# Kernel optimization log

Hardware: AMD Instinct MI355X
Metric: run time of the kernel (lower is better)

## Reference

```python
import jax, jax.numpy as jnp
import numpy as np

H = 8          # num_heads
CHUNK = 68     # tokens_per_chunk = blocks_per_chunk(4) * tokens_per_block(17)
EPS = 1e-5


def _layer_norm(t, w, b):
    m = t.mean(-1, keepdims=True)
    v = t.var(-1, keepdims=True)
    return (t - m) / jnp.sqrt(v + EPS) * w + b


def _forward(tokens, embedding, Wq, bq, Wk, bk, Wv, bv, Wg, bg, Wo, bo,
             gn_w, gn_b, ln1_w, ln1_b, ln2_w, ln2_b, w1, b1, w2, b2):
    B, S = tokens.shape
    L, D, _ = Wq.shape
    dh = D // H
    n_chunks = S // CHUNK

    x = embedding[tokens]  # [B,S,D]

    # per-head decay gammas (standard RetNet)
    gamma = 1.0 - 2.0 ** (-5.0 - jnp.arange(H, dtype=jnp.float32))  # [H]

    # rotary relative-position tables (absolute positions, fresh state n=0)
    pos = jnp.arange(S, dtype=jnp.float32)
    inv = 1.0 / (10000.0 ** (jnp.arange(0, dh, 2, dtype=jnp.float32) / dh))
    ang = pos[:, None] * inv[None, :]                      # [S, dh/2]
    cs = jnp.concatenate([jnp.cos(ang)] * 2, -1)[None, :, None, :]  # [1,S,1,dh]
    sn = jnp.concatenate([jnp.sin(ang)] * 2, -1)[None, :, None, :]

    def rot(t):  # t: [B,S,H,dh]
        t1, t2 = jnp.split(t, 2, axis=-1)
        return t * cs + jnp.concatenate([-t2, t1], -1) * sn

    # chunkwise decay structures
    idx = jnp.arange(CHUNK, dtype=jnp.float32)
    expo = idx[:, None] - idx[None, :]
    Dmask = jnp.where(expo >= 0, gamma[:, None, None] ** expo[None], 0.0)  # [H,C,C]
    cross_dec = gamma[None, :] ** (idx[:, None] + 1.0)          # [C,H]
    k_dec = gamma[None, :] ** (CHUNK - 1.0 - idx[:, None])      # [C,H]
    chunk_dec = gamma ** CHUNK                                  # [H]

    for l in range(L):
        h = _layer_norm(x, ln1_w[l], ln1_b[l])
        q = rot((h @ Wq[l] + bq[l]).reshape(B, S, H, dh))
        k = rot((h @ Wk[l] + bk[l]).reshape(B, S, H, dh)) * (dh ** -0.5)
        v = (h @ Wv[l] + bv[l]).reshape(B, S, H, dh)
        # split into chunks, scan carries the per-head KV state [B,H,dh,dh]
        qc = q.reshape(B, n_chunks, CHUNK, H, dh).transpose(1, 0, 2, 3, 4)
        kc = k.reshape(B, n_chunks, CHUNK, H, dh).transpose(1, 0, 2, 3, 4)
        vc = v.reshape(B, n_chunks, CHUNK, H, dh).transpose(1, 0, 2, 3, 4)

        def step(state, qkv):
            qq, kk, vv = qkv  # each [B,C,H,dh]
            inner = jnp.einsum('bihd,bjhd->bhij', qq, kk) * Dmask
            out = jnp.einsum('bhij,bjhd->bihd', inner, vv)
            out = out + jnp.einsum('bihd,bhde->bihe', qq, state) * cross_dec[None, :, :, None]
            state = state * chunk_dec[None, :, None, None] + \
                jnp.einsum('bjhd,bjhe->bhde', kk * k_dec[None, :, :, None], vv)
            return state, out

        state0 = jnp.zeros((B, H, dh, dh), dtype=x.dtype)
        _, ret = jax.lax.scan(step, state0, (qc, kc, vc))
        ret = ret.transpose(1, 0, 2, 3, 4).reshape(B, S, H, dh)
        # per-head group norm
        m = ret.mean(-1, keepdims=True)
        vr = ret.var(-1, keepdims=True)
        ret = (ret - m) / jnp.sqrt(vr + EPS)
        ret = (ret * gn_w[l].reshape(H, dh) + gn_b[l].reshape(H, dh)).reshape(B, S, D)
        g = jax.nn.silu(h @ Wg[l] + bg[l])
        x = x + (g * ret) @ Wo[l] + bo[l]
        h2 = _layer_norm(x, ln2_w[l], ln2_b[l])
        x = x + jax.nn.silu(h2 @ w1[l] + b1[l]) @ w2[l] + b2[l]
    return x


def setup_inputs() -> dict:
    key = jax.random.key(0)
    B, S, D, L, FF, V = 16, 408, 512, 10, 2048, 519
    ks = jax.random.split(key, 16)
    r = lambda i, shape, s=0.02: jax.random.normal(ks[i], shape, dtype=jnp.float32) * s
    return {
        'tokens': jax.random.randint(ks[0], (B, S), 0, V, dtype=jnp.int32),
        'embedding': r(1, (V, D)),
        'Wq': r(2, (L, D, D)), 'bq': jnp.zeros((L, D), jnp.float32),
        'Wk': r(3, (L, D, D)), 'bk': jnp.zeros((L, D), jnp.float32),
        'Wv': r(4, (L, D, D)), 'bv': jnp.zeros((L, D), jnp.float32),
        'Wg': r(5, (L, D, D)), 'bg': jnp.zeros((L, D), jnp.float32),
        'Wo': r(6, (L, D, D)), 'bo': jnp.zeros((L, D), jnp.float32),
        'gn_w': jnp.ones((L, D), jnp.float32), 'gn_b': jnp.zeros((L, D), jnp.float32),
        'ln1_w': jnp.ones((L, D), jnp.float32), 'ln1_b': jnp.zeros((L, D), jnp.float32),
        'ln2_w': jnp.ones((L, D), jnp.float32), 'ln2_b': jnp.zeros((L, D), jnp.float32),
        'w1': r(7, (L, D, FF)), 'b1': jnp.zeros((L, FF), jnp.float32),
        'w2': r(8, (L, FF, D)), 'b2': jnp.zeros((L, D), jnp.float32),
    }


def reference(tokens, embedding, Wq, bq, Wk, bk, Wv, bv, Wg, bg, Wo, bo,
              gn_w, gn_b, ln1_w, ln1_b, ln2_w, ln2_b, w1, b1, w2, b2):
    return _forward(tokens, embedding, Wq, bq, Wk, bk, Wv, bv, Wg, bg, Wo, bo,
                    gn_w, gn_b, ln1_w, ln1_b, ln2_w, ln2_b, w1, b1, w2, b2)
```

## Files before the change

### kernel.cpp

```cpp
#include <hip/hip_runtime.h>
#include <hip/hip_bf16.h>

#define H 8
#define DH 64
#define DMODEL 512
#define SEQ 408
#define BATCH 16
#define NLAYER 10
#define FFDIM 2048
#define CHUNK 68
#define NCHUNK 6
#define M (BATCH*SEQ)
#define EPS 1e-5f

typedef __hip_bfloat16 bf16;
typedef unsigned short ushort_t;
typedef short bf8v __attribute__((ext_vector_type(8)));
typedef float f4v  __attribute__((ext_vector_type(4)));

static constexpr size_t QKVG_STRIDE = 2u*512*512;
static constexpr size_t QKVG_HL     = 512*512;
static constexpr size_t WO_HI = 0;
static constexpr size_t WO_LO = WO_HI + 512*512;
static constexpr size_t W1_HI = WO_LO + 512*512;
static constexpr size_t W1_LO = W1_HI + 2048*512;
static constexpr size_t W2_HI = W1_LO + 2048*512;
static constexpr size_t W2_LO = W2_HI + 512*2048;

__device__ __forceinline__ float us2f(unsigned short u){ return __uint_as_float(((unsigned)u) << 16); }
__device__ __forceinline__ unsigned short f2bfs(float f){
  __bf16 h = (__bf16)f;
  return *(unsigned short*)&h;
}
__device__ __forceinline__ void split2(float f, unsigned short& hi, unsigned short& lo){
  hi = f2bfs(f);
  lo = f2bfs(f - us2f(hi));
}

__device__ __forceinline__ int xcd_swz(int fid, int nwg){
  int q = nwg >> 3;
  return (fid & 7) * q + (fid >> 3);
}

__global__ void embed_kernel(const int* __restrict__ tokens, const float* __restrict__ emb,
                             float* __restrict__ x){
  int idx = blockIdx.x*256 + threadIdx.x;
  if (idx >= M*DMODEL) return;
  int r = idx >> 9; int d = idx & 511;
  x[idx] = emb[(size_t)tokens[r]*DMODEL + d];
}

__global__ __launch_bounds__(256) void ln_kernel(const float* __restrict__ x,
    const float* __restrict__ w, const float* __restrict__ b,
    ushort_t* __restrict__ hhi, ushort_t* __restrict__ hlo){
  __shared__ float red[8];
  int r = blockIdx.x, tid = threadIdx.x;
  size_t base = (size_t)r*DMODEL;
  float v0 = x[base + tid], v1 = x[base + tid + 256];
  float s = v0 + v1, s2 = v0*v0 + v1*v1;
  int lane = tid & 63, wv = tid >> 6;
  #pragma unroll
  for (int o = 32; o; o >>= 1){ s += __shfl_xor(s, o); s2 += __shfl_xor(s2, o); }
  if (lane == 0){ red[wv] = s; red[wv+4] = s2; }
  __syncthreads();
  float tot  = red[0]+red[1]+red[2]+red[3];
  float tot2 = red[4]+red[5]+red[6]+red[7];
  float mean = tot * (1.0f/512.0f);
  float var  = tot2 * (1.0f/512.0f) - mean*mean;
  float rinv = rsqrtf(var + EPS);
  float o0 = (v0-mean)*rinv*w[tid]     + b[tid];
  float o1 = (v1-mean)*rinv*w[tid+256] + b[tid+256];
  unsigned short hi, lo;
  split2(o0, hi, lo); hhi[base+tid] = hi; hlo[base+tid] = lo;
  split2(o1, hi, lo); hhi[base+tid+256] = hi; hlo[base+tid+256] = lo;
}

__device__ __forceinline__ void wsplit_tile(const float* __restrict__ W,
    ushort_t* __restrict__ hi, ushort_t* __restrict__ lo,
    int N, int K, int n0, int k0)
{
  __shared__ float tb[32][33];
  int tx = threadIdx.x & 31, ty = threadIdx.x >> 5;
  #pragma unroll
  for (int r = 0; r < 32; r += 8)
    tb[ty+r][tx] = W[(size_t)(k0+ty+r)*N + n0 + tx];
  __syncthreads();
  #pragma unroll
  for (int r = 0; r < 32; r += 8){
    float v = tb[tx][ty+r];
    unsigned short h, l; split2(v, h, l);
    size_t o = (size_t)(n0+ty+r)*K + k0 + tx;
    hi[o] = h; lo[o] = l;
  }
}

__global__ __launch_bounds__(256) void wsplit_qkvg_kernel(
    const float* __restrict__ Wq, const float* __restrict__ Wk,
    const float* __restrict__ Wv, const float* __restrict__ Wg,
    ushort_t* __restrict__ wsp)
{
  int z = blockIdx.z;
  const float* W = (z==0)?Wq:(z==1)?Wk:(z==2)?Wv:Wg;
  ushort_t* hi = wsp + (size_t)z*QKVG_STRIDE;
  wsplit_tile(W, hi, hi + QKVG_HL, 512, 512, blockIdx.x*32, blockIdx.y*32);
}

__global__ __launch_bounds__(256) void wsplit_ffo_kernel(
    const float* __restrict__ Wo, const float* __restrict__ w1,
    const float* __restrict__ w2, ushort_t* __restrict__ wsp)
{
  int b = blockIdx.x;
  const float* W; ushort_t* hi; int N, K, n0, k0;
  if (b < 256){
    W = Wo; hi = wsp + WO_HI; N = 512; K = 512;
    n0 = (b & 15)*32; k0 = (b >> 4)*32;
  } else if (b < 1280){
    int bb = b - 256;
    W = w1; hi = wsp + W1_HI; N = 2048; K = 512;
    n0 = (bb & 63)*32; k0 = (bb >> 6)*32;
  } else {
    int bb = b - 1280;
    W = w2; hi = wsp + W2_HI; N = 512; K = 2048;
    n0 = (bb & 15)*32; k0 = (bb >> 4)*32;
  }
  wsplit_tile(W, hi, hi + (size_t)N*K, N, K, n0, k0);
}

#define BK 32
#define LDK 40

template<int TBM, int TBN>
__global__ __launch_bounds__(256) void gemm_ps_kernel(
    const ushort_t* __restrict__ Ahi, const ushort_t* __restrict__ Alo,
    const ushort_t* __restrict__ Bhi, const ushort_t* __restrict__ Blo,
    const float* __restrict__ bias,
    const float* Cin, float* Cout, ushort_t* Co_hi, ushort_t* Co_lo,
    int N, int K, int epi)
{
  constexpr int TMi = TBM/32;
  constexpr int TNj = TBN/32;
  __shared__ __align__(16) short AsH[TBM*LDK];
  __shared__ __align__(16) short AsL[TBM*LDK];
  __shared__ __align__(16) short BsH[TBN*LDK];
  __shared__ __align__(16) short BsL[TBN*LDK];
  int tid = threadIdx.x;
  int lane = tid & 63, wave = tid >> 6;
  int wm = (wave >> 1) * (TBM/2), wn = (wave & 1) * (TBN/2);
  int l15 = lane & 15, quad = lane >> 4;

  int nwg = gridDim.x * gridDim.y;
  int fid = blockIdx.y * gridDim.x + blockIdx.x;
  int swz = xcd_swz(fid, nwg);
  int bn = (swz % gridDim.x) * TBN;
  int bm = (swz / gridDim.x) * TBM;

  f4v acc[TMi][TNj];
  #pragma unroll
  for (int i = 0; i < TMi; i++)
    #pragma unroll
    for (int j = 0; j < TNj; j++) acc[i][j] = (f4v){0.f,0.f,0.f,0.f};

  int arow, akseg, bnn, bkseg;
  if (TBM == 128){ arow = tid >> 1; akseg = (tid & 1) * 16; }
  else           { arow = tid >> 2; akseg = (tid & 3) * 8;  }
  if (TBN == 128){ bnn = tid & 127; bkseg = (tid >> 7) * 16; }
  else           { bnn = tid & 63;  bkseg = (tid >> 6) * 8;  }

  const ushort_t* aH = Ahi + (size_t)(bm + arow)*K + akseg;
  const ushort_t* aL = Alo + (size_t)(bm + arow)*K + akseg;
  const ushort_t* bH = Bhi + (size_t)(bn + bnn)*K + bkseg;
  const ushort_t* bL = Blo + (size_t)(bn + bnn)*K + bkseg;

  uint4 rAh0, rAh1, rAl0, rAl1, rBh0, rBh1, rBl0, rBl1;
#define GLOAD_PS(k0) do{ \
    rAh0 = *(const uint4*)(aH + (k0)); \
    rAl0 = *(const uint4*)(aL + (k0)); \
    if (TBM == 128){ rAh1 = *(const uint4*)(aH + (k0) + 8); \
                     rAl1 = *(const uint4*)(aL + (k0) + 8); } \
    rBh0 = *(const uint4*)(bH + (k0)); \
    rBl0 = *(const uint4*)(bL + (k0)); \
    if (TBN == 128){ rBh1 = *(const uint4*)(bH + (k0) + 8); \
                     rBl1 = *(const uint4*)(bL + (k0) + 8); } \
  }while(0)

  GLOAD_PS(0);
  const int nt = K / BK;
  for (int t = 0; t < nt; t++){
    __syncthreads();
    *(uint4*)&AsH[arow*LDK + akseg] = rAh0;
    *(uint4*)&AsL[arow*LDK + akseg] = rAl0;
    if (TBM == 128){
      *(uint4*)&AsH[arow*LDK + akseg + 8] = rAh1;
      *(uint4*)&AsL[arow*LDK + akseg + 8] = rAl1;
    }
    *(uint4*)&BsH[bnn*LDK + bkseg] = rBh0;
    *(uint4*)&BsL[bnn*LDK + bkseg] = rBl0;
    if (TBN == 128){
      *(uint4*)&BsH[bnn*LDK + bkseg + 8] = rBh1;
      *(uint4*)&BsL[bnn*LDK + bkseg + 8] = rBl1;
    }
    __syncthreads();
    if (t + 1 < nt) GLOAD_PS((t+1)*BK);
    bf8v afh[TMi], afl[TMi], bfh[TNj], bfl[TNj];
    #pragma unroll
    for (int i = 0; i < TMi; i++){
      afh[i] = *(const bf8v*)&AsH[(wm + i*16 + l15)*LDK + quad*8];
      afl[i] = *(const bf8v*)&AsL[(wm + i*16 + l15)*LDK + quad*8];
    }
    #pragma unroll
    for (int j = 0; j < TNj; j++){
      bfh[j] = *(const bf8v*)&BsH[(wn + j*16 + l15)*LDK + quad*8];
      bfl[j] = *(const bf8v*)&BsL[(wn + j*16 + l15)*LDK + quad*8];
    }
    #pragma unroll
    for (int i = 0; i < TMi; i++)
      #pragma unroll
      for (int j = 0; j < TNj; j++){
        acc[i][j] = __builtin_amdgcn_mfma_f32_16x16x32_bf16(afh[i], bfl[j], acc[i][j], 0, 0, 0);
        acc[i][j] = __builtin_amdgcn_mfma_f32_16x16x32_bf16(afl[i], bfh[j], acc[i][j], 0, 0, 0);
        acc[i][j] = __builtin_amdgcn_mfma_f32_16x16x32_bf16(afh[i], bfh[j], acc[i][j], 0, 0, 0);
      }
  }
#undef GLOAD_PS
  #pragma unroll
  for (int i = 0; i < TMi; i++){
    int m0 = bm + wm + i*16 + quad*4;
    #pragma unroll
    for (int j = 0; j < TNj; j++){
      int n = bn + wn + j*16 + l15;
      float bsv = bias[n];
      #pragma unroll
      for (int r = 0; r < 4; r++){
        int m = m0 + r;
        float c = acc[i][j][r] + bsv;
        if (epi == 1) c = c / (1.0f + expf(-c));
        if (epi == 2) c += Cin[(size_t)m*N + n];
        if (Co_hi){
          unsigned short hi, lo; split2(c, hi, lo);
          Co_hi[(size_t)m*N + n] = hi;
          Co_lo[(size_t)m*N + n] = lo;
        } else {
          Cout[(size_t)m*N + n] = c;
        }
      }
    }
  }
}

__global__ __launch_bounds__(256) void gemm_qkvg_kernel(
    const ushort_t* __restrict__ Ahi, const ushort_t* __restrict__ Alo,
    const ushort_t* __restrict__ wsp,
    const float* __restrict__ bq, const float* __restrict__ bk,
    const float* __restrict__ bv, const float* __restrict__ bg,
    float* __restrict__ qo, float* __restrict__ ko,
    float* __restrict__ vo, float* __restrict__ go)
{
  const int N = DMODEL, K = DMODEL;
  __shared__ __align__(16) short AsH[128*LDK];
  __shared__ __align__(16) short AsL[128*LDK];
  __shared__ __align__(16) short BsH[128*LDK];
  __shared__ __align__(16) short BsL[128*LDK];
  int tid = threadIdx.x;
  int lane = tid & 63, wave = tid >> 6;
  int wm = (wave >> 1) * 64, wn = (wave & 1) * 64;
  int l15 = lane & 15, quad = lane >> 4;

  int nwg = gridDim.x * gridDim.y;
  int fid = blockIdx.y * gridDim.x + blockIdx.x;
  int swz = xcd_swz(fid, nwg);
  int bx = swz % gridDim.x;
  int which = bx >> 2;
  int bn = (bx & 3) * 128;
  int bm = (swz / gridDim.x) * 128;

  const ushort_t* Bhi = wsp + (size_t)which * QKVG_STRIDE;
  const ushort_t* Blo = Bhi + QKVG_HL;
  const float* bias = (which==0) ? bq : (which==1) ? bk : (which==2) ? bv : bg;
  float* out        = (which==0) ? qo : (which==1) ? ko : (which==2) ? vo : go;

  f4v acc[4][4];
  #pragma unroll
  for (int i = 0; i < 4; i++)
    #pragma unroll
    for (int j = 0; j < 4; j++) acc[i][j] = (f4v){0.f,0.f,0.f,0.f};

  int arow = tid >> 1, akseg = (tid & 1) * 16;
  int bnn = tid & 127, bkseg = (tid >> 7) * 16;

  const ushort_t* aH = Ahi + (size_t)(bm + arow)*K + akseg;
  const ushort_t* aL = Alo + (size_t)(bm + arow)*K + akseg;
  const ushort_t* bH = Bhi + (size_t)(bn + bnn)*K + bkseg;
  const ushort_t* bL = Blo + (size_t)(bn + bnn)*K + bkseg;

  uint4 rAh0, rAh1, rAl0, rAl1, rBh0, rBh1, rBl0, rBl1;
#define GLOADQ(k0) do{ \
    rAh0 = *(const uint4*)(aH + (k0)); rAh1 = *(const uint4*)(aH + (k0) + 8); \
    rAl0 = *(const uint4*)(aL + (k0)); rAl1 = *(const uint4*)(aL + (k0) + 8); \
    rBh0 = *(const uint4*)(bH + (k0)); rBh1 = *(const uint4*)(bH + (k0) + 8); \
    rBl0 = *(const uint4*)(bL + (k0)); rBl1 = *(const uint4*)(bL + (k0) + 8); \
  }while(0)

  GLOADQ(0);
  const int nt = K / BK;
  for (int t = 0; t < nt; t++){
    __syncthreads();
    *(uint4*)&AsH[arow*LDK + akseg]     = rAh0;
    *(uint4*)&AsH[arow*LDK + akseg + 8] = rAh1;
    *(uint4*)&AsL[arow*LDK + akseg]     = rAl0;
    *(uint4*)&AsL[arow*LDK + akseg + 8] = rAl1;
    *(uint4*)&BsH[bnn*LDK + bkseg] = rBh0; *(uint4*)&BsH[bnn*LDK + bkseg + 8] = rBh1;
    *(uint4*)&BsL[bnn*LDK + bkseg] = rBl0; *(uint4*)&BsL[bnn*LDK + bkseg + 8] = rBl1;
    __syncthreads();
    if (t + 1 < nt) GLOADQ((t+1)*BK);
    bf8v afh[4], afl[4], bfh[4], bfl[4];
    #pragma unroll
    for (int i = 0; i < 4; i++){
      afh[i] = *(const bf8v*)&AsH[(wm + i*16 + l15)*LDK + quad*8];
      afl[i] = *(const bf8v*)&AsL[(wm + i*16 + l15)*LDK + quad*8];
      bfh[i] = *(const bf8v*)&BsH[(wn + i*16 + l15)*LDK + quad*8];
      bfl[i] = *(const bf8v*)&BsL[(wn + i*16 + l15)*LDK + quad*8];
    }
    #pragma unroll
    for (int i = 0; i < 4; i++)
      #pragma unroll
      for (int j = 0; j < 4; j++){
        acc[i][j] = __builtin_amdgcn_mfma_f32_16x16x32_bf16(afh[i], bfl[j], acc[i][j], 0, 0, 0);
        acc[i][j] = __builtin_amdgcn_mfma_f32_16x16x32_bf16(afl[i], bfh[j], acc[i][j], 0, 0, 0);
        acc[i][j] = __builtin_amdgcn_mfma_f32_16x16x32_bf16(afh[i], bfh[j], acc[i][j], 0, 0, 0);
      }
  }
#undef GLOADQ
  #pragma unroll
  for (int i = 0; i < 4; i++){
    int m0 = bm + wm + i*16 + quad*4;
    #pragma unroll
    for (int j = 0; j < 4; j++){
      int n = bn + wn + j*16 + l15;
      float bsv = bias[n];
      #pragma unroll
      for (int r = 0; r < 4; r++){
        int m = m0 + r;
        float c = acc[i][j][r] + bsv;
        if (which == 3) c = c / (1.0f + expf(-c));
        out[(size_t)m*N + n] = c;
      }
    }
  }
}

__global__ void rope_kernel(float* __restrict__ q, float* __restrict__ k){
  int idx = blockIdx.x*256 + threadIdx.x;
  if (idx >= M*256) return;
  int r = idx >> 8, p = idx & 255;
  int hh = p >> 5, i = p & 31;
  int s = r % SEQ;
  float inv = powf(10000.0f, -(float)(2*i) * (1.0f/64.0f));
  float ang = (float)s * inv;
  float sn, c; sincosf(ang, &sn, &c);
  size_t base = (size_t)r*DMODEL + hh*64 + i;
  float q1 = q[base], q2 = q[base+32];
  q[base]    = q1*c - q2*sn;
  q[base+32] = q2*c + q1*sn;
  float k1 = k[base], k2 = k[base+32];
  const float sc = 0.125f;
  k[base]    = (k1*c - k2*sn)*sc;
  k[base+32] = (k2*c + k1*sn)*sc;
}

__global__ __launch_bounds__(256) void ret_chunkkv_kernel(
    const float* __restrict__ k, const float* __restrict__ v, float* __restrict__ Ast)
{
  __shared__ __align__(16) float kT[DH][CHUNK];
  __shared__ __align__(16) float vs[CHUNK][DH];
  __shared__ float gpw[CHUNK];
  int tid = threadIdx.x;
  int c = blockIdx.x % NCHUNK;
  int bh = blockIdx.x / NCHUNK;
  int hh = bh & 7, b = bh >> 3;
  float gamma = 1.0f - exp2f(-5.0f - (float)hh);
  if (tid < CHUNK) gpw[tid] = powf(gamma, (float)(CHUNK-1-tid));
  size_t rowbase = ((size_t)(b*SEQ + c*CHUNK))*DMODEL + hh*DH;
  for (int e = tid; e < CHUNK*DH; e += 256){
    int i = e >> 6, d = e & 63;
    size_t g = rowbase + (size_t)i*DMODEL + d;
    kT[d][i] = k[g];
    vs[i][d] = v[g];
  }
  __syncthreads();
  float* A = Ast + (size_t)blockIdx.x * (DH*DH);
  for (int e = tid; e < DH*16; e += 256){
    int d = e >> 4, q4 = (e & 15) * 4;
    float4 a4 = {0,0,0,0};
    for (int j = 0; j < CHUNK; j++){
      float kj = kT[d][j] * gpw[j];
      float4 v4 = *(const float4*)&vs[j][q4];
      a4.x += kj*v4.x; a4.y += kj*v4.y; a4.z += kj*v4.z; a4.w += kj*v4.w;
    }
    *(float4*)&A[d*DH + q4] = a4;
  }
}

__global__ __launch_bounds__(256) void ret_scan_kernel(float* __restrict__ Ast)
{
  int bh = blockIdx.x, hh = bh & 7;
  float gamma = 1.0f - exp2f(-5.0f - (float)hh);
  float chdec = powf(gamma, (float)CHUNK);
  int tid = threadIdx.x;
  float4 run[4];
  #pragma unroll
  for (int t = 0; t < 4; t++) run[t] = (float4){0,0,0,0};
  size_t base = (size_t)bh * NCHUNK * (DH*DH) + (size_t)tid*16;
  for (int c = 0; c < NCHUNK; c++){
    float4* slot = (float4*)(Ast + base + (size_t)c*(DH*DH));
    float4 a[4];
    #pragma unroll
    for (int t = 0; t < 4; t++) a[t] = slot[t];
    #pragma unroll
    for (int t = 0; t < 4; t++) slot[t] = run[t];
    #pragma unroll
    for (int t = 0; t < 4; t++){
      run[t].x = run[t].x*chdec + a[t].x;
      run[t].y = run[t].y*chdec + a[t].y;
      run[t].z = run[t].z*chdec + a[t].z;
      run[t].w = run[t].w*chdec + a[t].w;
    }
  }
}

__global__ __launch_bounds__(256) void ret_out_kernel(
    const float* __restrict__ q, const float* __restrict__ k, const float* __restrict__ v,
    const float* __restrict__ Ast, float* __restrict__ ret)
{
  __shared__ __align__(16) float qs[CHUNK][DH];
  __shared__ __align__(16) float kT[DH][CHUNK];
  __shared__ __align__(16) float vs[CHUNK][DH];
  __shared__ __align__(16) float sts[DH*DH];
  __shared__ float inner[34][CHUNK];
  __shared__ float gpw[CHUNK];
  int tid = threadIdx.x;
  int c = blockIdx.x % NCHUNK;
  int bh = blockIdx.x / NCHUNK;
  int hh = bh & 7, b = bh >> 3;
  float gamma = 1.0f - exp2f(-5.0f - (float)hh);
  if (tid < CHUNK) gpw[tid] = powf(gamma, (float)tid);
  size_t rowbase = ((size_t)(b*SEQ + c*CHUNK))*DMODEL + hh*DH;
  for (int e = tid; e < CHUNK*DH; e += 256){
    int i = e >> 6, d = e & 63;
    size_t g = rowbase + (size_t)i*DMODEL + d;
    qs[i][d] = q[g];
    kT[d][i] = k[g];
    vs[i][d] = v[g];
  }
  const float* st = Ast + (size_t)blockIdx.x * (DH*DH);
  for (int e = tid*4; e < DH*DH; e += 1024)
    *(float4*)&sts[e] = *(const float4*)&st[e];
  __syncthreads();
  for (int p = 0; p < 2; p++){
    int i0 = p*34;
    for (int e = tid; e < 34*CHUNK; e += 256){
      int ii = e / CHUNK, j = e - ii*CHUNK;
      int i = i0 + ii;
      float val = 0.0f;
      if (j <= i){
        float dot = 0.0f;
        #pragma unroll 16
        for (int d = 0; d < DH; d++) dot += qs[i][d] * kT[d][j];
        val = dot * gpw[i-j];
      }
      inner[ii][j] = val;
    }
    __syncthreads();
    for (int e = tid; e < 34*16; e += 256){
      int ii = e >> 4, q4 = (e & 15) * 4;
      int i = i0 + ii;
      float4 o4 = {0,0,0,0};
      for (int j = 0; j <= i; j++){
        float w = inner[ii][j];
        float4 v4 = *(const float4*)&vs[j][q4];
        o4.x += w*v4.x; o4.y += w*v4.y; o4.z += w*v4.z; o4.w += w*v4.w;
      }
      float4 c4 = {0,0,0,0};
      #pragma unroll 8
      for (int e2 = 0; e2 < DH; e2++){
        float qv = qs[i][e2];
        float4 s4 = *(const float4*)&sts[e2*DH + q4];
        c4.x += qv*s4.x; c4.y += qv*s4.y; c4.z += qv*s4.z; c4.w += qv*s4.w;
      }
      float cd = gpw[i] * gamma;
      size_t ob = rowbase + (size_t)i*DMODEL + q4;
      float4 o; o.x = o4.x + cd*c4.x; o.y = o4.y + cd*c4.y;
      o.z = o4.z + cd*c4.z; o.w = o4.w + cd*c4.w;
      *(float4*)&ret[ob] = o;
    }
    __syncthreads();
  }
}

__global__ __launch_bounds__(512) void gnorm_gate_kernel(const float* __restrict__ ret,
    const float* __restrict__ g, const float* __restrict__ gnw, const float* __restrict__ gnb,
    ushort_t* __restrict__ ohi, ushort_t* __restrict__ olo)
{
  int r = blockIdx.x, tid = threadIdx.x;
  size_t idx = (size_t)r*DMODEL + tid;
  float val = ret[idx];
  float s = val, s2 = val*val;
  #pragma unroll
  for (int o = 32; o; o >>= 1){ s += __shfl_xor(s, o); s2 += __shfl_xor(s2, o); }
  float mean = s * (1.0f/64.0f);
  float var  = s2 * (1.0f/64.0f) - mean*mean;
  float y = (val - mean) * rsqrtf(var + EPS);
  y = y * gnw[tid] + gnb[tid];
  y = y * g[idx];
  unsigned short hi, lo; split2(y, hi, lo);
  ohi[idx] = hi; olo[idx] = lo;
}

__global__ void outwrite_kernel(const float* __restrict__ x, float* __restrict__ out){
  int idx = blockIdx.x*256 + threadIdx.x;
  if (idx < M*DMODEL) out[idx] = x[idx];
}

extern "C" void kernel_launch(void* const* d_in, const int* in_sizes, int n_in,
                              void* d_out, int out_size, void* d_ws, size_t ws_size,
                              hipStream_t stream)
{
  (void)in_sizes; (void)n_in; (void)out_size; (void)ws_size;
  const int*   tokens = (const int*)d_in[0];
  const float* emb  = (const float*)d_in[1];
  const float* Wq = (const float*)d_in[2];  const float* bq = (const float*)d_in[3];
  const float* Wk = (const float*)d_in[4];  const float* bk = (const float*)d_in[5];
  const float* Wv = (const float*)d_in[6];  const float* bv = (const float*)d_in[7];
  const float* Wg = (const float*)d_in[8];  const float* bg = (const float*)d_in[9];
  const float* Wo = (const float*)d_in[10]; const float* bo = (const float*)d_in[11];
  const float* gnw = (const float*)d_in[12]; const float* gnb = (const float*)d_in[13];
  const float* ln1w = (const float*)d_in[14]; const float* ln1b = (const float*)d_in[15];
  const float* ln2w = (const float*)d_in[16]; const float* ln2b = (const float*)d_in[17];
  const float* w1 = (const float*)d_in[18]; const float* b1 = (const float*)d_in[19];
  const float* w2 = (const float*)d_in[20]; const float* b2 = (const float*)d_in[21];

  const size_t MD = (size_t)M*DMODEL;
  float* xf = (float*)d_ws;
  float* qf = xf + MD;
  float* kf = qf + MD;
  float* vf = kf + MD;
  float* gf = vf + MD;
  float* rf = gf + MD;
  ushort_t* h_hi = (ushort_t*)(rf + MD);
  ushort_t* h_lo = h_hi + MD;
  float* Ast = (float*)h_hi;
  ushort_t* rg_hi = h_hi;
  ushort_t* rg_lo = h_lo;
  ushort_t* ff_hi = (ushort_t*)qf;
  ushort_t* ff_lo = (ushort_t*)vf;
  ushort_t* wsp = (ushort_t*)rf;

  embed_kernel<<<(M*DMODEL)/256, 256, 0, stream>>>(tokens, emb, xf);

  dim3 gqkvg(16, M/128);
  dim3 g64(DMODEL/64, M/64);
  dim3 gff(FFDIM/128, M/128);
  dim3 gsplit4(16, 16, 4);
  for (int l = 0; l < NLAYER; l++){
    const size_t wO = (size_t)l*DMODEL*DMODEL;
    const size_t bO = (size_t)l*DMODEL;
    const size_t w1O = (size_t)l*DMODEL*FFDIM;
    const size_t b1O = (size_t)l*FFDIM;
    wsplit_qkvg_kernel<<<gsplit4, 256, 0, stream>>>(Wq + wO, Wk + wO, Wv + wO, Wg + wO, wsp);
    ln_kernel<<<M, 256, 0, stream>>>(xf, ln1w + bO, ln1b + bO, h_hi, h_lo);
    gemm_qkvg_kernel<<<gqkvg, 256, 0, stream>>>(h_hi, h_lo, wsp,
        bq + bO, bk + bO, bv + bO, bg + bO,
        qf, kf, vf, gf);
    rope_kernel<<<M, 256, 0, stream>>>(qf, kf);
    ret_chunkkv_kernel<<<BATCH*H*NCHUNK, 256, 0, stream>>>(kf, vf, Ast);
    ret_scan_kernel<<<BATCH*H, 256, 0, stream>>>(Ast);
    ret_out_kernel<<<BATCH*H*NCHUNK, 256, 0, stream>>>(qf, kf, vf, Ast, rf);
    gnorm_gate_kernel<<<M, 512, 0, stream>>>(rf, gf, gnw + bO, gnb + bO, rg_hi, rg_lo);
    wsplit_ffo_kernel<<<2304, 256, 0, stream>>>(Wo + wO, w1 + w1O, w2 + w1O, wsp);
    gemm_ps_kernel<64,64><<<g64, 256, 0, stream>>>(rg_hi, rg_lo,
        wsp + WO_HI, wsp + WO_LO, bo + bO, xf, xf, nullptr, nullptr, DMODEL, DMODEL, 2);
    ln_kernel<<<M, 256, 0, stream>>>(xf, ln2w + bO, ln2b + bO, h_hi, h_lo);
    gemm_ps_kernel<128,128><<<gff, 256, 0, stream>>>(h_hi, h_lo,
        wsp + W1_HI, wsp + W1_LO, b1 + b1O, nullptr, nullptr, ff_hi, ff_lo, FFDIM, DMODEL, 1);
    gemm_ps_kernel<64,64><<<g64, 256, 0, stream>>>(ff_hi, ff_lo,
        wsp + W2_HI, wsp + W2_LO, b2 + bO, xf, xf, nullptr, nullptr, DMODEL, FFDIM, 2);
  }
  outwrite_kernel<<<(M*DMODEL)/256, 256, 0, stream>>>(xf, (float*)d_out);
}
```

Measured before the change: 4.145 ms.

## Stage GEMM tiles via direct global-to-LDS loads with double buffering

The split-bf16 GEMM kernels (QKVG and the generic projection GEMM) now copy operand tiles straight from global memory into double-buffered LDS using global_load_lds 16-byte transfers. This replaces the register-staged loads and the second barrier per K step. All these GEMMs also move to one 64x128 tile shape without LDS padding, with launch grids updated to match. The aim is to overlap the next tile's load with the MFMA work and save VGPRs and LDS store instructions. The risks are LDS bank conflicts from the unpadded rows, different occupancy and wave counts per GEMM, and needing correct vmcnt waits before the single barrier.

```diff
diff --git a/kernel.cpp b/kernel.cpp
--- a/kernel.cpp
+++ b/kernel.cpp
@@ -35,6 +35,12 @@
 __device__ __forceinline__ void split2(float f, unsigned short& hi, unsigned short& lo){
   hi = f2bfs(f);
   lo = f2bfs(f - us2f(hi));
+}
+
+typedef const __attribute__((address_space(1))) unsigned int* gas_ptr;
+typedef __attribute__((address_space(3))) unsigned int* las_ptr;
+__device__ __forceinline__ void gld16(const void* g, void* l){
+  __builtin_amdgcn_global_load_lds((gas_ptr)g, (las_ptr)l, 16, 0, 0);
 }
 
 __device__ __forceinline__ int xcd_swz(int fid, int nwg){
@@ -127,9 +133,16 @@
 }
 
 #define BK 32
-#define LDK 40
-
-template<int TBM, int TBN>
+
+#define STAGE_PS(buf, kofs) do{ \
+    gld16(aHp + (kofs), &AsH[buf][tid*8]); \
+    gld16(aLp + (kofs), &AsL[buf][tid*8]); \
+    gld16(bHp + (kofs), &BsH[buf][tid*8]); \
+    gld16(bLp + (kofs), &BsL[buf][tid*8]); \
+    gld16(bHp2 + (kofs), &BsH[buf][tid*8 + 2048]); \
+    gld16(bLp2 + (kofs), &BsL[buf][tid*8 + 2048]); \
+  }while(0)
+
 __global__ __launch_bounds__(256) void gemm_ps_kernel(
     const ushort_t* __restrict__ Ahi, const ushort_t* __restrict__ Alo,
     const ushort_t* __restrict__ Bhi, const ushort_t* __restrict__ Blo,
@@ -137,96 +150,66 @@
     const float* Cin, float* Cout, ushort_t* Co_hi, ushort_t* Co_lo,
     int N, int K, int epi)
 {
-  constexpr int TMi = TBM/32;
-  constexpr int TNj = TBN/32;
-  __shared__ __align__(16) short AsH[TBM*LDK];
-  __shared__ __align__(16) short AsL[TBM*LDK];
-  __shared__ __align__(16) short BsH[TBN*LDK];
-  __shared__ __align__(16) short BsL[TBN*LDK];
+  __shared__ __align__(16) short AsH[2][64*BK];
+  __shared__ __align__(16) short AsL[2][64*BK];
+  __shared__ __align__(16) short BsH[2][128*BK];
+  __shared__ __align__(16) short BsL[2][128*BK];
   int tid = threadIdx.x;
   int lane = tid & 63, wave = tid >> 6;
-  int wm = (wave >> 1) * (TBM/2), wn = (wave & 1) * (TBN/2);
+  int wm = (wave >> 1) * 32, wn = (wave & 1) * 64;
   int l15 = lane & 15, quad = lane >> 4;
 
   int nwg = gridDim.x * gridDim.y;
   int fid = blockIdx.y * gridDim.x + blockIdx.x;
   int swz = xcd_swz(fid, nwg);
-  int bn = (swz % gridDim.x) * TBN;
-  int bm = (swz / gridDim.x) * TBM;
-
-  f4v acc[TMi][TNj];
-  #pragma unroll
-  for (int i = 0; i < TMi; i++)
-    #pragma unroll
-    for (int j = 0; j < TNj; j++) acc[i][j] = (f4v){0.f,0.f,0.f,0.f};
-
-  int arow, akseg, bnn, bkseg;
-  if (TBM == 128){ arow = tid >> 1; akseg = (tid & 1) * 16; }
-  else           { arow = tid >> 2; akseg = (tid & 3) * 8;  }
-  if (TBN == 128){ bnn = tid & 127; bkseg = (tid >> 7) * 16; }
-  else           { bnn = tid & 63;  bkseg = (tid >> 6) * 8;  }
-
-  const ushort_t* aH = Ahi + (size_t)(bm + arow)*K + akseg;
-  const ushort_t* aL = Alo + (size_t)(bm + arow)*K + akseg;
-  const ushort_t* bH = Bhi + (size_t)(bn + bnn)*K + bkseg;
-  const ushort_t* bL = Blo + (size_t)(bn + bnn)*K + bkseg;
-
-  uint4 rAh0, rAh1, rAl0, rAl1, rBh0, rBh1, rBl0, rBl1;
-#define GLOAD_PS(k0) do{ \
-    rAh0 = *(const uint4*)(aH + (k0)); \
-    rAl0 = *(const uint4*)(aL + (k0)); \
-    if (TBM == 128){ rAh1 = *(const uint4*)(aH + (k0) + 8); \
-                     rAl1 = *(const uint4*)(aL + (k0) + 8); } \
-    rBh0 = *(const uint4*)(bH + (k0)); \
-    rBl0 = *(const uint4*)(bL + (k0)); \
-    if (TBN == 128){ rBh1 = *(const uint4*)(bH + (k0) + 8); \
-                     rBl1 = *(const uint4*)(bL + (k0) + 8); } \
-  }while(0)
-
-  GLOAD_PS(0);
+  int bn = (swz % gridDim.x) * 128;
+  int bm = (swz / gridDim.x) * 64;
+
+  f4v acc[2][4];
+  #pragma unroll
+  for (int i = 0; i < 2; i++)
+    #pragma unroll
+    for (int j = 0; j < 4; j++) acc[i][j] = (f4v){0.f,0.f,0.f,0.f};
+
+  int arow = tid >> 2, ak = (tid & 3) * 8;
+  const ushort_t* aHp  = Ahi + (size_t)(bm + arow)*K + ak;
+  const ushort_t* aLp  = Alo + (size_t)(bm + arow)*K + ak;
+  const ushort_t* bHp  = Bhi + (size_t)(bn + arow)*K + ak;
+  const ushort_t* bLp  = Blo + (size_t)(bn + arow)*K + ak;
+  const ushort_t* bHp2 = Bhi + (size_t)(bn + 64 + arow)*K + ak;
+  const ushort_t* bLp2 = Blo + (size_t)(bn + 64 + arow)*K + ak;
+
+  STAGE_PS(0, 0);
   const int nt = K / BK;
   for (int t = 0; t < nt; t++){
     __syncthreads();
-    *(uint4*)&AsH[arow*LDK + akseg] = rAh0;
-    *(uint4*)&AsL[arow*LDK + akseg] = rAl0;
-    if (TBM == 128){
-      *(uint4*)&AsH[arow*LDK + akseg + 8] = rAh1;
-      *(uint4*)&AsL[arow*LDK + akseg + 8] = rAl1;
-    }
-    *(uint4*)&BsH[bnn*LDK + bkseg] = rBh0;
-    *(uint4*)&BsL[bnn*LDK + bkseg] = rBl0;
-    if (TBN == 128){
-      *(uint4*)&BsH[bnn*LDK + bkseg + 8] = rBh1;
-      *(uint4*)&BsL[bnn*LDK + bkseg + 8] = rBl1;
-    }
-    __syncthreads();
-    if (t + 1 < nt) GLOAD_PS((t+1)*BK);
-    bf8v afh[TMi], afl[TMi], bfh[TNj], bfl[TNj];
-    #pragma unroll
-    for (int i = 0; i < TMi; i++){
-      afh[i] = *(const bf8v*)&AsH[(wm + i*16 + l15)*LDK + quad*8];
-      afl[i] = *(const bf8v*)&AsL[(wm + i*16 + l15)*LDK + quad*8];
-    }
-    #pragma unroll
-    for (int j = 0; j < TNj; j++){
-      bfh[j] = *(const bf8v*)&BsH[(wn + j*16 + l15)*LDK + quad*8];
-      bfl[j] = *(const bf8v*)&BsL[(wn + j*16 + l15)*LDK + quad*8];
-    }
-    #pragma unroll
-    for (int i = 0; i < TMi; i++)
+    if (t + 1 < nt) STAGE_PS((t+1)&1, (t+1)*BK);
+    int cur = t & 1;
+    bf8v afh[2], afl[2], bfh[4], bfl[4];
+    #pragma unroll
+    for (int i = 0; i < 2; i++){
+      afh[i] = *(const bf8v*)&AsH[cur][(wm + i*16 + l15)*BK + quad*8];
+      afl[i] = *(const bf8v*)&AsL[cur][(wm + i*16 + l15)*BK + quad*8];
+    }
+    #pragma unroll
+    for (int j = 0; j < 4; j++){
+      bfh[j] = *(const bf8v*)&BsH[cur][(wn + j*16 + l15)*BK + quad*8];
+      bfl[j] = *(const bf8v*)&BsL[cur][(wn + j*16 + l15)*BK + quad*8];
+    }
+    #pragma unroll
+    for (int i = 0; i < 2; i++)
       #pragma unroll
-      for (int j = 0; j < TNj; j++){
+      for (int j = 0; j < 4; j++){
         acc[i][j] = __builtin_amdgcn_mfma_f32_16x16x32_bf16(afh[i], bfl[j], acc[i][j], 0, 0, 0);
         acc[i][j] = __builtin_amdgcn_mfma_f32_16x16x32_bf16(afl[i], bfh[j], acc[i][j], 0, 0, 0);
         acc[i][j] = __builtin_amdgcn_mfma_f32_16x16x32_bf16(afh[i], bfh[j], acc[i][j], 0, 0, 0);
       }
   }
-#undef GLOAD_PS
-  #pragma unroll
-  for (int i = 0; i < TMi; i++){
+  #pragma unroll
+  for (int i = 0; i < 2; i++){
     int m0 = bm + wm + i*16 + quad*4;
     #pragma unroll
-    for (int j = 0; j < TNj; j++){
+    for (int j = 0; j < 4; j++){
       int n = bn + wn + j*16 + l15;
       float bsv = bias[n];
       #pragma unroll
@@ -256,13 +239,13 @@
     float* __restrict__ vo, float* __restrict__ go)
 {
   const int N = DMODEL, K = DMODEL;
-  __shared__ __align__(16) short AsH[128*LDK];
-  __shared__ __align__(16) short AsL[128*LDK];
-  __shared__ __align__(16) short BsH[128*LDK];
-  __shared__ __align__(16) short BsL[128*LDK];
+  __shared__ __align__(16) short AsH[2][64*BK];
+  __shared__ __align__(16) short AsL[2][64*BK];
+  __shared__ __align__(16) short BsH[2][128*BK];
+  __shared__ __align__(16) short BsL[2][128*BK];
   int tid = threadIdx.x;
   int lane = tid & 63, wave = tid >> 6;
-  int wm = (wave >> 1) * 64, wn = (wave & 1) * 64;
+  int wm = (wave >> 1) * 32, wn = (wave & 1) * 64;
   int l15 = lane & 15, quad = lane >> 4;
 
   int nwg = gridDim.x * gridDim.y;
@@ -271,57 +254,46 @@
   int bx = swz % gridDim.x;
   int which = bx >> 2;
   int bn = (bx & 3) * 128;
-  int bm = (swz / gridDim.x) * 128;
+  int bm = (swz / gridDim.x) * 64;
 
   const ushort_t* Bhi = wsp + (size_t)which * QKVG_STRIDE;
   const ushort_t* Blo = Bhi + QKVG_HL;
   const float* bias = (which==0) ? bq : (which==1) ? bk : (which==2) ? bv : bg;
   float* out        = (which==0) ? qo : (which==1) ? ko : (which==2) ? vo : go;
 
-  f4v acc[4][4];
-  #pragma unroll
-  for (int i = 0; i < 4; i++)
+  f4v acc[2][4];
+  #pragma unroll
+  for (int i = 0; i < 2; i++)
     #pragma unroll
     for (int j = 0; j < 4; j++) acc[i][j] = (f4v){0.f,0.f,0.f,0.f};
 
-  int arow = tid >> 1, akseg = (tid & 1) * 16;
-  int bnn = tid & 127, bkseg = (tid >> 7) * 16;
-
-  const ushort_t* aH = Ahi + (size_t)(bm + arow)*K + akseg;
-  const ushort_t* aL = Alo + (size_t)(bm + arow)*K + akseg;
-  const ushort_t* bH = Bhi + (size_t)(bn + bnn)*K + bkseg;
-  const ushort_t* bL = Blo + (size_t)(bn + bnn)*K + bkseg;
-
-  uint4 rAh0, rAh1, rAl0, rAl1, rBh0, rBh1, rBl0, rBl1;
-#define GLOADQ(k0) do{ \
-    rAh0 = *(const uint4*)(aH + (k0)); rAh1 = *(const uint4*)(aH + (k0) + 8); \
-    rAl0 = *(const uint4*)(aL + (k0)); rAl1 = *(const uint4*)(aL + (k0) + 8); \
-    rBh0 = *(const uint4*)(bH + (k0)); rBh1 = *(const uint4*)(bH + (k0) + 8); \
-    rBl0 = *(const uint4*)(bL + (k0)); rBl1 = *(const uint4*)(bL + (k0) + 8); \
-  }while(0)
-
-  GLOADQ(0);
+  int arow = tid >> 2, ak = (tid & 3) * 8;
+  const ushort_t* aHp  = Ahi + (size_t)(bm + arow)*K + ak;
+  const ushort_t* aLp  = Alo + (size_t)(bm + arow)*K + ak;
+  const ushort_t* bHp  = Bhi + (size_t)(bn + arow)*K + ak;
+  const ushort_t* bLp  = Blo + (size_t)(bn + arow)*K + ak;
+  const ushort_t* bHp2 = Bhi + (size_t)(bn + 64 + arow)*K + ak;
+  const ushort_t* bLp2 = Blo + (size_t)(bn + 64 + arow)*K + ak;
+
+  STAGE_PS(0, 0);
   const int nt = K / BK;
   for (int t = 0; t < nt; t++){
     __syncthreads();
-    *(uint4*)&AsH[arow*LDK + akseg]     = rAh0;
-    *(uint4*)&AsH[arow*LDK + akseg + 8] = rAh1;
-    *(uint4*)&AsL[arow*LDK + akseg]     = rAl0;
-    *(uint4*)&AsL[arow*LDK + akseg + 8] = rAl1;
-    *(uint4*)&BsH[bnn*LDK + bkseg] = rBh0; *(uint4*)&BsH[bnn*LDK + bkseg + 8] = rBh1;
-    *(uint4*)&BsL[bnn*LDK + bkseg] = rBl0; *(uint4*)&BsL[bnn*LDK + bkseg + 8] = rBl1;
-    __syncthreads();
-    if (t + 1 < nt) GLOADQ((t+1)*BK);
-    bf8v afh[4], afl[4], bfh[4], bfl[4];
-    #pragma unroll
-    for (int i = 0; i < 4; i++){
-      afh[i] = *(const bf8v*)&AsH[(wm + i*16 + l15)*LDK + quad*8];
-      afl[i] = *(const bf8v*)&AsL[(wm + i*16 + l15)*LDK + quad*8];
-      bfh[i] = *(const bf8v*)&BsH[(wn + i*16 + l15)*LDK + quad*8];
-      bfl[i] = *(const bf8v*)&BsL[(wn + i*16 + l15)*LDK + quad*8];
-    }
-    #pragma unroll
-    for (int i = 0; i < 4; i++)
+    if (t + 1 < nt) STAGE_PS((t+1)&1, (t+1)*BK);
+    int cur = t & 1;
+    bf8v afh[2], afl[2], bfh[4], bfl[4];
+    #pragma unroll
+    for (int i = 0; i < 2; i++){
+      afh[i] = *(const bf8v*)&AsH[cur][(wm + i*16 + l15)*BK + quad*8];
+      afl[i] = *(const bf8v*)&AsL[cur][(wm + i*16 + l15)*BK + quad*8];
+    }
+    #pragma unroll
+    for (int j = 0; j < 4; j++){
+      bfh[j] = *(const bf8v*)&BsH[cur][(wn + j*16 + l15)*BK + quad*8];
+      bfl[j] = *(const bf8v*)&BsL[cur][(wn + j*16 + l15)*BK + quad*8];
+    }
+    #pragma unroll
+    for (int i = 0; i < 2; i++)
       #pragma unroll
       for (int j = 0; j < 4; j++){
         acc[i][j] = __builtin_amdgcn_mfma_f32_16x16x32_bf16(afh[i], bfl[j], acc[i][j], 0, 0, 0);
@@ -329,9 +301,8 @@
         acc[i][j] = __builtin_amdgcn_mfma_f32_16x16x32_bf16(afh[i], bfh[j], acc[i][j], 0, 0, 0);
       }
   }
-#undef GLOADQ
-  #pragma unroll
-  for (int i = 0; i < 4; i++){
+  #pragma unroll
+  for (int i = 0; i < 2; i++){
     int m0 = bm + wm + i*16 + quad*4;
     #pragma unroll
     for (int j = 0; j < 4; j++){
@@ -556,9 +527,9 @@
 
   embed_kernel<<<(M*DMODEL)/256, 256, 0, stream>>>(tokens, emb, xf);
 
-  dim3 gqkvg(16, M/128);
-  dim3 g64(DMODEL/64, M/64);
-  dim3 gff(FFDIM/128, M/128);
+  dim3 gqkvg(16, M/64);
+  dim3 g512(DMODEL/128, M/64);
+  dim3 gff(FFDIM/128, M/64);
   dim3 gsplit4(16, 16, 4);
   for (int l = 0; l < NLAYER; l++){
     const size_t wO = (size_t)l*DMODEL*DMODEL;
@@ -576,12 +547,12 @@
     ret_out_kernel<<<BATCH*H*NCHUNK, 256, 0, stream>>>(qf, kf, vf, Ast, rf);
     gnorm_gate_kernel<<<M, 512, 0, stream>>>(rf, gf, gnw + bO, gnb + bO, rg_hi, rg_lo);
     wsplit_ffo_kernel<<<2304, 256, 0, stream>>>(Wo + wO, w1 + w1O, w2 + w1O, wsp);
-    gemm_ps_kernel<64,64><<<g64, 256, 0, stream>>>(rg_hi, rg_lo,
+    gemm_ps_kernel<<<g512, 256, 0, stream>>>(rg_hi, rg_lo,
         wsp + WO_HI, wsp + WO_LO, bo + bO, xf, xf, nullptr, nullptr, DMODEL, DMODEL, 2);
     ln_kernel<<<M, 256, 0, stream>>>(xf, ln2w + bO, ln2b + bO, h_hi, h_lo);
-    gemm_ps_kernel<128,128><<<gff, 256, 0, stream>>>(h_hi, h_lo,
+    gemm_ps_kernel<<<gff, 256, 0, stream>>>(h_hi, h_lo,
         wsp + W1_HI, wsp + W1_LO, b1 + b1O, nullptr, nullptr, ff_hi, ff_lo, FFDIM, DMODEL, 1);
-    gemm_ps_kernel<64,64><<<g64, 256, 0, stream>>>(ff_hi, ff_lo,
+    gemm_ps_kernel<<<g512, 256, 0, stream>>>(ff_hi, ff_lo,
         wsp + W2_HI, wsp + W2_LO, b2 + bO, xf, xf, nullptr, nullptr, DMODEL, FFDIM, 2);
   }
   outwrite_kernel<<<(M*DMODEL)/256, 256, 0, stream>>>(xf, (float*)d_out);
```

Result: faster. 3.767 ms (-9.1%).
